# Optimization experiments

Measured on AMD Instinct MI355X. Metric: run time of the kernel, lower is better.

## Reference

```python
import jax, jax.numpy as jnp
import numpy as np

B, NSL, DS = 8, 12, 768
L, R, DL = 24, 64, 4096
DP = 4096
DIM_T = NSL * 2 * DS          # 18432
FUSED = 1024 + 512            # 1536
GEN_IN = FUSED + 256 + 64     # 1856


def setup_inputs() -> dict:
    key = jax.random.key(0)
    ks = jax.random.split(key, 16)
    s = lambda d: 1.0 / np.sqrt(d)
    return {
        "A_small": jax.random.normal(ks[0], (B, NSL, 1, DS), jnp.float32),
        "B_small": jax.random.normal(ks[1], (B, NSL, DS, 1), jnp.float32),
        "prompt_emb": jax.random.normal(ks[2], (B, DP), jnp.float32),
        "W_ct": jax.random.normal(ks[3], (DIM_T, 1024), jnp.float32) * s(DIM_T),
        "b_ct": jnp.zeros((1024,), jnp.float32),
        "W_cp": jax.random.normal(ks[4], (DP, 512), jnp.float32) * s(DP),
        "b_cp": jnp.zeros((512,), jnp.float32),
        "W_pc": jax.random.normal(ks[5], (FUSED, L), jnp.float32) * s(FUSED),
        "b_pc": jnp.zeros((L,), jnp.float32),
        "E_layer": jax.random.normal(ks[6], (L, 256), jnp.float32),
        "E_chunk": jax.random.normal(ks[7], (R, 64), jnp.float32),
        "W_A": jax.random.normal(ks[8], (GEN_IN, DL), jnp.float32) * s(GEN_IN),
        "b_A": jnp.zeros((DL,), jnp.float32),
        "W_B": jax.random.normal(ks[9], (GEN_IN, DL), jnp.float32) * s(GEN_IN),
        "b_B": jnp.zeros((DL,), jnp.float32),
    }


def reference(A_small, B_small, prompt_emb, W_ct, b_ct, W_cp, b_cp, W_pc, b_pc,
              E_layer, E_chunk, W_A, b_A, W_B, b_B):
    bsz = prompt_emb.shape[0]
    flat_T = jnp.concatenate([A_small.reshape(bsz, -1), B_small.reshape(bsz, -1)], axis=-1)
    t_feat = jax.nn.relu(flat_T @ W_ct + b_ct)          # [B,1024]
    p_feat = jax.nn.relu(prompt_emb @ W_cp + b_cp)      # [B,512]
    fused = jnp.concatenate([t_feat, p_feat], axis=-1)  # [B,1536]
    logits = fused @ W_pc + b_pc                        # [B,L]
    y_soft = jax.nn.sigmoid(logits)                     # eval mode (no gumbel)
    y_hard = (y_soft > 0.5).astype(y_soft.dtype)
    gate = y_soft + jax.lax.stop_gradient(y_hard - y_soft)  # straight-through

    # Batched hypernetwork over all (layer, chunk) pairs instead of a double loop.
    ctx = jnp.broadcast_to(fused[:, None, None, :], (bsz, L, R, FUSED))
    le = jnp.broadcast_to(E_layer[None, :, None, :], (bsz, L, R, 256))
    ce = jnp.broadcast_to(E_chunk[None, None, :, :], (bsz, L, R, 64))
    gen = jnp.concatenate([ctx, le, ce], axis=-1)       # [B,L,R,1856]

    A = gen @ W_A + b_A                                 # [B,L,R,DL]
    Bm = gen @ W_B + b_B                                # [B,L,R,DL]
    A_large = A * gate[:, :, None, None]                # [B,L,R,DL]
    B_large = jnp.transpose(Bm, (0, 1, 3, 2))           # [B,L,DL,R]
    return (A_large, B_large, gate)
```

## Files before the change

kernel.cpp:

```cpp
#include <hip/hip_runtime.h>

typedef float v4f __attribute__((ext_vector_type(4)));

#define NB 8
#define NL 24
#define NR 64
#define ND 4096
#define NFUSED 1536
#define NTF 1024
#define NPF 512
#define KP 4096

#define TKC 144
#define PKC 32
#define FKC 12

#define WS_FUSED 0
#define WS_GATE  12288
#define WS_PLA   12480
#define WS_PLB   209088
#define WS_CA    405696
#define WS_CBT   667840
#define WS_PT    929984
#define WS_PP    2109632
#define WS_PFA   2240704
#define WS_PFB   2633920

__global__ __launch_bounds__(256) void k_indep(
    const float* __restrict__ As, const float* __restrict__ Bs,
    const float* __restrict__ W_ct,
    const float* __restrict__ prompt, const float* __restrict__ W_cp,
    const float* __restrict__ E_layer, const float* __restrict__ E_chunk,
    const float* __restrict__ W_A, const float* __restrict__ W_B,
    float* __restrict__ partT, float* __restrict__ partP,
    float* __restrict__ pLA, float* __restrict__ pLB,
    float* __restrict__ CA, float* __restrict__ CBT) {
  __shared__ float e[NR * 64];
  const int bx = blockIdx.x;
  const int tid = threadIdx.x;

  if (bx < 576) {
    const int j = (bx & 3) * 256 + tid;
    const int kc = bx >> 2;
    const int kbase = kc * 128;
    float acc[NB] = {};
    for (int kk = 0; kk < 128; ++kk) {
      const int k = kbase + kk;
      const float w = W_ct[(size_t)k * NTF + j];
      const float* x = (k < 9216) ? (As + k) : (Bs + (k - 9216));
#pragma unroll
      for (int b = 0; b < NB; ++b) acc[b] = fmaf(x[b * 9216], w, acc[b]);
    }
#pragma unroll
    for (int b = 0; b < NB; ++b)
      partT[(size_t)(kc * NB + b) * NTF + j] = acc[b];
  } else if (bx < 640) {
    const int t = bx - 576;
    const int j = (t & 1) * 256 + tid;
    const int kc = t >> 1;
    const int kbase = kc * 128;
    float acc[NB] = {};
    for (int kk = 0; kk < 128; ++kk) {
      const int k = kbase + kk;
      const float w = W_cp[(size_t)k * NPF + j];
#pragma unroll
      for (int b = 0; b < NB; ++b) acc[b] = fmaf(prompt[b * KP + k], w, acc[b]);
    }
#pragma unroll
    for (int b = 0; b < NB; ++b)
      partP[(size_t)(kc * NB + b) * NPF + j] = acc[b];
  } else if (bx < 704) {
    const int t = bx - 640;
    const bool isA = t < 32;
    const int tt = isA ? t : t - 32;
    const int dc = tt & 15;
    const int kh = tt >> 4;
    const float* W = (isA ? W_A : W_B) + (size_t)(NFUSED + kh * 128) * ND;
    float* pL = (isA ? pLA : pLB) + (size_t)kh * NL * ND;
    const int d = dc * 256 + tid;
    float acc[NL] = {};
    for (int kk = 0; kk < 128; ++kk) {
      const float w = W[(size_t)kk * ND + d];
      const float* el = E_layer + kh * 128 + kk;
#pragma unroll
      for (int l = 0; l < NL; ++l) acc[l] = fmaf(el[l * 256], w, acc[l]);
    }
#pragma unroll
    for (int l = 0; l < NL; ++l) pL[(size_t)l * ND + d] = acc[l];
  } else {
    const int t = bx - 704;
    const bool isA = t < 16;
    const int tt = isA ? t : t - 16;
    const float* W = (isA ? W_A : W_B) + (size_t)(NFUSED + 256) * ND;
    for (int i = tid; i < NR * 64; i += 256) e[i] = E_chunk[i];
    __syncthreads();
    const int d = tt * 256 + tid;
    float w[64];
#pragma unroll
    for (int k = 0; k < 64; ++k) w[k] = W[(size_t)k * ND + d];
    for (int r = 0; r < NR; ++r) {
      float s = 0.f;
#pragma unroll
      for (int k = 0; k < 64; ++k) s = fmaf(e[r * 64 + k], w[k], s);
      if (isA) CA[(size_t)r * ND + d] = s;
      else     CBT[(size_t)d * NR + r] = s;
    }
  }
}

__global__ __launch_bounds__(256) void k_fused_reduce(
    const float* __restrict__ partT, const float* __restrict__ partP,
    const float* __restrict__ b_ct, const float* __restrict__ b_cp,
    float* __restrict__ fused) {
  const int bx = blockIdx.x;
  if (bx < 32) {
    const int idx = bx * 256 + threadIdx.x;
    const int b = idx >> 10, j = idx & 1023;
    float s = b_ct[j];
    for (int kc = 0; kc < TKC; ++kc) s += partT[(size_t)(kc * NB + b) * NTF + j];
    fused[b * NFUSED + j] = fmaxf(s, 0.f);
  } else {
    const int idx = (bx - 32) * 256 + threadIdx.x;
    const int b = idx >> 9, j = idx & 511;
    float s = b_cp[j];
    for (int kc = 0; kc < PKC; ++kc) s += partP[(size_t)(kc * NB + b) * NPF + j];
    fused[b * NFUSED + NTF + j] = fmaxf(s, 0.f);
  }
}

__global__ __launch_bounds__(256) void k_dep(
    const float* __restrict__ fused,
    const float* __restrict__ W_A, const float* __restrict__ W_B,
    const float* __restrict__ W_pc, const float* __restrict__ b_pc,
    float* __restrict__ pFA, float* __restrict__ pFB,
    float* __restrict__ gate_ws, float* __restrict__ gate_out) {
  __shared__ float red[256];
  const int bx = blockIdx.x;
  const int tid = threadIdx.x;
  if (bx < 384) {
    const bool isA = bx < 192;
    const int t = isA ? bx : bx - 192;
    const float* W = isA ? W_A : W_B;
    float* part = isA ? pFA : pFB;
    const int d = (t & 15) * 256 + tid;
    const int kc = t >> 4;
    const int kbase = kc * 128;
    float acc[NB] = {};
    for (int kk = 0; kk < 128; ++kk) {
      const int k = kbase + kk;
      const float w = W[(size_t)k * ND + d];
#pragma unroll
      for (int b = 0; b < NB; ++b) acc[b] = fmaf(fused[b * NFUSED + k], w, acc[b]);
    }
#pragma unroll
    for (int b = 0; b < NB; ++b)
      part[(size_t)(kc * NB + b) * ND + d] = acc[b];
  } else {
    const int bl = bx - 384;
    const int b = bl / NL, l = bl % NL;
    float s = 0.f;
    for (int k = tid; k < NFUSED; k += 256)
      s = fmaf(fused[b * NFUSED + k], W_pc[k * NL + l], s);
    red[tid] = s;
    __syncthreads();
#pragma unroll
    for (int off = 128; off > 0; off >>= 1) {
      if (tid < off) red[tid] += red[tid + off];
      __syncthreads();
    }
    if (tid == 0) {
      const float g = (red[0] + b_pc[l]) > 0.f ? 1.f : 0.f;
      gate_ws[bl] = g;
      gate_out[bl] = g;
    }
  }
}

__global__ __launch_bounds__(256) void k_out(
    const float* __restrict__ pFA, const float* __restrict__ pFB,
    const float* __restrict__ b_A, const float* __restrict__ b_B,
    const float* __restrict__ pLA, const float* __restrict__ pLB,
    const float* __restrict__ CA, const float* __restrict__ CBT,
    const float* __restrict__ gate,
    float* __restrict__ outA, float* __restrict__ outB) {
  __shared__ float sbase[512];
  const int bx = blockIdx.x;
  const int tid = threadIdx.x;
  if (bx < 1536) {
    const int bl = bx >> 3;
    const int rest = bx & 7;
    const int b = bl / NL, l = bl % NL;
    const int d = (rest >> 1) * 1024 + tid * 4;
    const int r0 = (rest & 1) * 32;
    const float g = gate[bl];
    v4f base = *(const v4f*)(b_A + d);
#pragma unroll
    for (int kc = 0; kc < FKC; ++kc)
      base += *(const v4f*)(pFA + (size_t)(kc * NB + b) * ND + d);
    base += *(const v4f*)(pLA + (size_t)l * ND + d);
    base += *(const v4f*)(pLA + (size_t)(NL + l) * ND + d);
    float* outp = outA + ((size_t)bl * NR + r0) * ND + d;
#pragma unroll 4
    for (int r = 0; r < 32; ++r) {
      const v4f c = *(const v4f*)(CA + (size_t)(r0 + r) * ND + d);
      const v4f v = (base + c) * g;
      __builtin_nontemporal_store(v, (v4f*)outp);
      outp += ND;
    }
  } else {
    const int t = bx - 1536;
    const int bl = t >> 3;
    const int b = bl / NL, l = bl % NL;
    const int dbase = (t & 7) * 512;
    for (int dd = tid; dd < 512; dd += 256) {
      const int d = dbase + dd;
      float s = b_B[d] + pLB[(size_t)l * ND + d] + pLB[(size_t)(NL + l) * ND + d];
#pragma unroll
      for (int kc = 0; kc < FKC; ++kc)
        s += pFB[(size_t)(kc * NB + b) * ND + d];
      sbase[dd] = s;
    }
    __syncthreads();
    const int dd16 = tid >> 4;
    const int r4 = (tid & 15) * 4;
#pragma unroll 4
    for (int i = 0; i < 32; ++i) {
      const int dloc = i * 16 + dd16;
      const int d = dbase + dloc;
      const v4f c = *(const v4f*)(CBT + (size_t)d * NR + r4);
      const v4f v = c + sbase[dloc];
      __builtin_nontemporal_store(v, (v4f*)(outB + ((size_t)bl * ND + d) * NR + r4));
    }
  }
}

extern "C" void kernel_launch(void* const* d_in, const int* in_sizes, int n_in,
                              void* d_out, int out_size, void* d_ws, size_t ws_size,
                              hipStream_t stream) {
  const float* A_small   = (const float*)d_in[0];
  const float* B_small   = (const float*)d_in[1];
  const float* prompt    = (const float*)d_in[2];
  const float* W_ct      = (const float*)d_in[3];
  const float* b_ct      = (const float*)d_in[4];
  const float* W_cp      = (const float*)d_in[5];
  const float* b_cp      = (const float*)d_in[6];
  const float* W_pc      = (const float*)d_in[7];
  const float* b_pc      = (const float*)d_in[8];
  const float* E_layer   = (const float*)d_in[9];
  const float* E_chunk   = (const float*)d_in[10];
  const float* W_A       = (const float*)d_in[11];
  const float* b_A       = (const float*)d_in[12];
  const float* W_B       = (const float*)d_in[13];
  const float* b_B       = (const float*)d_in[14];

  float* ws    = (float*)d_ws;
  float* fused = ws + WS_FUSED;
  float* gatew = ws + WS_GATE;
  float* pLA   = ws + WS_PLA;
  float* pLB   = ws + WS_PLB;
  float* CA    = ws + WS_CA;
  float* CBT   = ws + WS_CBT;
  float* partT = ws + WS_PT;
  float* partP = ws + WS_PP;
  float* pFA   = ws + WS_PFA;
  float* pFB   = ws + WS_PFB;

  float* outA = (float*)d_out;
  float* outB = outA + (size_t)192 * NR * ND;
  float* outG = outB + (size_t)192 * ND * NR;

  k_indep<<<736, 256, 0, stream>>>(A_small, B_small, W_ct, prompt, W_cp,
                                   E_layer, E_chunk, W_A, W_B,
                                   partT, partP, pLA, pLB, CA, CBT);
  k_fused_reduce<<<48, 256, 0, stream>>>(partT, partP, b_ct, b_cp, fused);
  k_dep<<<576, 256, 0, stream>>>(fused, W_A, W_B, W_pc, b_pc,
                                 pFA, pFB, gatew, outG);
  k_out<<<3072, 256, 0, stream>>>(pFA, pFB, b_A, b_B, pLA, pLB, CA, CBT,
                                  gatew, outA, outB);
}
```

Before: 151.5 us.

## Merge four kernels into one persistent cooperative kernel with grid syncs

Replaces the four separate kernel launches with a single cooperative persistent kernel. Each former kernel's block range becomes a grid-stride loop over work units, and grid.sync() separates the stages. This removes the launch gaps and inter-kernel drain between the stages. The cost is that the grid is capped by occupancy (at most 1024 blocks), each grid barrier carries overhead, and the launch_bounds(256,4) register cap may cause spills in the register-heavy stages.

Result: slower. 521.4 us (+244.2%).

```diff
diff --git a/kernel.cpp b/kernel.cpp
--- a/kernel.cpp
+++ b/kernel.cpp
@@ -1,4 +1,7 @@
 #include <hip/hip_runtime.h>
+#include <hip/hip_cooperative_groups.h>
+
+namespace cg = cooperative_groups;
 
 typedef float v4f __attribute__((ext_vector_type(4)));
 
@@ -26,210 +29,198 @@
 #define WS_PFA   2240704
 #define WS_PFB   2633920
 
-__global__ __launch_bounds__(256) void k_indep(
-    const float* __restrict__ As, const float* __restrict__ Bs,
-    const float* __restrict__ W_ct,
-    const float* __restrict__ prompt, const float* __restrict__ W_cp,
-    const float* __restrict__ E_layer, const float* __restrict__ E_chunk,
-    const float* __restrict__ W_A, const float* __restrict__ W_B,
-    float* __restrict__ partT, float* __restrict__ partP,
-    float* __restrict__ pLA, float* __restrict__ pLB,
-    float* __restrict__ CA, float* __restrict__ CBT) {
-  __shared__ float e[NR * 64];
-  const int bx = blockIdx.x;
+struct KParams {
+  const float *As, *Bs, *prompt, *W_ct, *b_ct, *W_cp, *b_cp, *W_pc, *b_pc,
+              *E_layer, *E_chunk, *W_A, *b_A, *W_B, *b_B;
+  float *fused, *gatew, *pLA, *pLB, *CA, *CBT, *partT, *partP, *pFA, *pFB;
+  float *outA, *outB, *outG;
+};
+
+__global__ __launch_bounds__(256, 4) void k_all(KParams p) {
+  cg::grid_group grid = cg::this_grid();
+  const int bid = blockIdx.x;
   const int tid = threadIdx.x;
-
-  if (bx < 576) {
-    const int j = (bx & 3) * 256 + tid;
-    const int kc = bx >> 2;
-    const int kbase = kc * 128;
-    float acc[NB] = {};
-    for (int kk = 0; kk < 128; ++kk) {
-      const int k = kbase + kk;
-      const float w = W_ct[(size_t)k * NTF + j];
-      const float* x = (k < 9216) ? (As + k) : (Bs + (k - 9216));
-#pragma unroll
-      for (int b = 0; b < NB; ++b) acc[b] = fmaf(x[b * 9216], w, acc[b]);
-    }
-#pragma unroll
-    for (int b = 0; b < NB; ++b)
-      partT[(size_t)(kc * NB + b) * NTF + j] = acc[b];
-  } else if (bx < 640) {
-    const int t = bx - 576;
-    const int j = (t & 1) * 256 + tid;
-    const int kc = t >> 1;
-    const int kbase = kc * 128;
-    float acc[NB] = {};
-    for (int kk = 0; kk < 128; ++kk) {
-      const int k = kbase + kk;
-      const float w = W_cp[(size_t)k * NPF + j];
-#pragma unroll
-      for (int b = 0; b < NB; ++b) acc[b] = fmaf(prompt[b * KP + k], w, acc[b]);
-    }
-#pragma unroll
-    for (int b = 0; b < NB; ++b)
-      partP[(size_t)(kc * NB + b) * NPF + j] = acc[b];
-  } else if (bx < 704) {
-    const int t = bx - 640;
-    const bool isA = t < 32;
-    const int tt = isA ? t : t - 32;
-    const int dc = tt & 15;
-    const int kh = tt >> 4;
-    const float* W = (isA ? W_A : W_B) + (size_t)(NFUSED + kh * 128) * ND;
-    float* pL = (isA ? pLA : pLB) + (size_t)kh * NL * ND;
-    const int d = dc * 256 + tid;
-    float acc[NL] = {};
-    for (int kk = 0; kk < 128; ++kk) {
-      const float w = W[(size_t)kk * ND + d];
-      const float* el = E_layer + kh * 128 + kk;
-#pragma unroll
-      for (int l = 0; l < NL; ++l) acc[l] = fmaf(el[l * 256], w, acc[l]);
-    }
-#pragma unroll
-    for (int l = 0; l < NL; ++l) pL[(size_t)l * ND + d] = acc[l];
-  } else {
-    const int t = bx - 704;
-    const bool isA = t < 16;
-    const int tt = isA ? t : t - 16;
-    const float* W = (isA ? W_A : W_B) + (size_t)(NFUSED + 256) * ND;
-    for (int i = tid; i < NR * 64; i += 256) e[i] = E_chunk[i];
-    __syncthreads();
-    const int d = tt * 256 + tid;
-    float w[64];
-#pragma unroll
-    for (int k = 0; k < 64; ++k) w[k] = W[(size_t)k * ND + d];
-    for (int r = 0; r < NR; ++r) {
+  const int G = gridDim.x;
+  __shared__ float smem[4096];
+
+  for (int u = bid; u < 736; u += G) {
+    if (u < 576) {
+      const int j = (u & 3) * 256 + tid;
+      const int kc = u >> 2;
+      const int kbase = kc * 128;
+      float acc[NB] = {};
+      for (int kk = 0; kk < 128; ++kk) {
+        const int k = kbase + kk;
+        const float w = p.W_ct[(size_t)k * NTF + j];
+        const float* x = (k < 9216) ? (p.As + k) : (p.Bs + (k - 9216));
+#pragma unroll
+        for (int b = 0; b < NB; ++b) acc[b] = fmaf(x[b * 9216], w, acc[b]);
+      }
+#pragma unroll
+      for (int b = 0; b < NB; ++b)
+        p.partT[(size_t)(kc * NB + b) * NTF + j] = acc[b];
+    } else if (u < 640) {
+      const int t = u - 576;
+      const int j = (t & 1) * 256 + tid;
+      const int kc = t >> 1;
+      const int kbase = kc * 128;
+      float acc[NB] = {};
+      for (int kk = 0; kk < 128; ++kk) {
+        const int k = kbase + kk;
+        const float w = p.W_cp[(size_t)k * NPF + j];
+#pragma unroll
+        for (int b = 0; b < NB; ++b) acc[b] = fmaf(p.prompt[b * KP + k], w, acc[b]);
+      }
+#pragma unroll
+      for (int b = 0; b < NB; ++b)
+        p.partP[(size_t)(kc * NB + b) * NPF + j] = acc[b];
+    } else if (u < 704) {
+      const int t = u - 640;
+      const bool isA = t < 32;
+      const int tt = isA ? t : t - 32;
+      const int dc = tt & 15;
+      const int kh = tt >> 4;
+      const float* W = (isA ? p.W_A : p.W_B) + (size_t)(NFUSED + kh * 128) * ND;
+      float* pL = (isA ? p.pLA : p.pLB) + (size_t)kh * NL * ND;
+      const int d = dc * 256 + tid;
+      float acc[NL] = {};
+      for (int kk = 0; kk < 128; ++kk) {
+        const float w = W[(size_t)kk * ND + d];
+        const float* el = p.E_layer + kh * 128 + kk;
+#pragma unroll
+        for (int l = 0; l < NL; ++l) acc[l] = fmaf(el[l * 256], w, acc[l]);
+      }
+#pragma unroll
+      for (int l = 0; l < NL; ++l) pL[(size_t)l * ND + d] = acc[l];
+    } else {
+      const int t = u - 704;
+      const bool isA = t < 16;
+      const int tt = isA ? t : t - 16;
+      const float* W = (isA ? p.W_A : p.W_B) + (size_t)(NFUSED + 256) * ND;
+      __syncthreads();
+      for (int i = tid; i < NR * 64; i += 256) smem[i] = p.E_chunk[i];
+      __syncthreads();
+      const int d = tt * 256 + tid;
+      float w[64];
+#pragma unroll
+      for (int k = 0; k < 64; ++k) w[k] = W[(size_t)k * ND + d];
+      for (int r = 0; r < NR; ++r) {
+        float s = 0.f;
+#pragma unroll
+        for (int k = 0; k < 64; ++k) s = fmaf(smem[r * 64 + k], w[k], s);
+        if (isA) p.CA[(size_t)r * ND + d] = s;
+        else     p.CBT[(size_t)d * NR + r] = s;
+      }
+    }
+  }
+  grid.sync();
+
+  for (int u = bid; u < 48; u += G) {
+    if (u < 32) {
+      const int idx = u * 256 + tid;
+      const int b = idx >> 10, j = idx & 1023;
+      float s = p.b_ct[j];
+      for (int kc = 0; kc < TKC; ++kc) s += p.partT[(size_t)(kc * NB + b) * NTF + j];
+      p.fused[b * NFUSED + j] = fmaxf(s, 0.f);
+    } else {
+      const int idx = (u - 32) * 256 + tid;
+      const int b = idx >> 9, j = idx & 511;
+      float s = p.b_cp[j];
+      for (int kc = 0; kc < PKC; ++kc) s += p.partP[(size_t)(kc * NB + b) * NPF + j];
+      p.fused[b * NFUSED + NTF + j] = fmaxf(s, 0.f);
+    }
+  }
+  grid.sync();
+
+  for (int u = bid; u < 576; u += G) {
+    if (u < 384) {
+      const bool isA = u < 192;
+      const int t = isA ? u : u - 192;
+      const float* W = isA ? p.W_A : p.W_B;
+      float* part = isA ? p.pFA : p.pFB;
+      const int d = (t & 15) * 256 + tid;
+      const int kc = t >> 4;
+      const int kbase = kc * 128;
+      float acc[NB] = {};
+      for (int kk = 0; kk < 128; ++kk) {
+        const int k = kbase + kk;
+        const float w = W[(size_t)k * ND + d];
+#pragma unroll
+        for (int b = 0; b < NB; ++b) acc[b] = fmaf(p.fused[b * NFUSED + k], w, acc[b]);
+      }
+#pragma unroll
+      for (int b = 0; b < NB; ++b)
+        part[(size_t)(kc * NB + b) * ND + d] = acc[b];
+    } else {
+      const int bl = u - 384;
+      const int b = bl / NL, l = bl % NL;
       float s = 0.f;
-#pragma unroll
-      for (int k = 0; k < 64; ++k) s = fmaf(e[r * 64 + k], w[k], s);
-      if (isA) CA[(size_t)r * ND + d] = s;
-      else     CBT[(size_t)d * NR + r] = s;
-    }
-  }
-}
-
-__global__ __launch_bounds__(256) void k_fused_reduce(
-    const float* __restrict__ partT, const float* __restrict__ partP,
-    const float* __restrict__ b_ct, const float* __restrict__ b_cp,
-    float* __restrict__ fused) {
-  const int bx = blockIdx.x;
-  if (bx < 32) {
-    const int idx = bx * 256 + threadIdx.x;
-    const int b = idx >> 10, j = idx & 1023;
-    float s = b_ct[j];
-    for (int kc = 0; kc < TKC; ++kc) s += partT[(size_t)(kc * NB + b) * NTF + j];
-    fused[b * NFUSED + j] = fmaxf(s, 0.f);
-  } else {
-    const int idx = (bx - 32) * 256 + threadIdx.x;
-    const int b = idx >> 9, j = idx & 511;
-    float s = b_cp[j];
-    for (int kc = 0; kc < PKC; ++kc) s += partP[(size_t)(kc * NB + b) * NPF + j];
-    fused[b * NFUSED + NTF + j] = fmaxf(s, 0.f);
-  }
-}
-
-__global__ __launch_bounds__(256) void k_dep(
-    const float* __restrict__ fused,
-    const float* __restrict__ W_A, const float* __restrict__ W_B,
-    const float* __restrict__ W_pc, const float* __restrict__ b_pc,
-    float* __restrict__ pFA, float* __restrict__ pFB,
-    float* __restrict__ gate_ws, float* __restrict__ gate_out) {
-  __shared__ float red[256];
-  const int bx = blockIdx.x;
-  const int tid = threadIdx.x;
-  if (bx < 384) {
-    const bool isA = bx < 192;
-    const int t = isA ? bx : bx - 192;
-    const float* W = isA ? W_A : W_B;
-    float* part = isA ? pFA : pFB;
-    const int d = (t & 15) * 256 + tid;
-    const int kc = t >> 4;
-    const int kbase = kc * 128;
-    float acc[NB] = {};
-    for (int kk = 0; kk < 128; ++kk) {
-      const int k = kbase + kk;
-      const float w = W[(size_t)k * ND + d];
-#pragma unroll
-      for (int b = 0; b < NB; ++b) acc[b] = fmaf(fused[b * NFUSED + k], w, acc[b]);
-    }
-#pragma unroll
-    for (int b = 0; b < NB; ++b)
-      part[(size_t)(kc * NB + b) * ND + d] = acc[b];
-  } else {
-    const int bl = bx - 384;
-    const int b = bl / NL, l = bl % NL;
-    float s = 0.f;
-    for (int k = tid; k < NFUSED; k += 256)
-      s = fmaf(fused[b * NFUSED + k], W_pc[k * NL + l], s);
-    red[tid] = s;
-    __syncthreads();
-#pragma unroll
-    for (int off = 128; off > 0; off >>= 1) {
-      if (tid < off) red[tid] += red[tid + off];
-      __syncthreads();
-    }
-    if (tid == 0) {
-      const float g = (red[0] + b_pc[l]) > 0.f ? 1.f : 0.f;
-      gate_ws[bl] = g;
-      gate_out[bl] = g;
-    }
-  }
-}
-
-__global__ __launch_bounds__(256) void k_out(
-    const float* __restrict__ pFA, const float* __restrict__ pFB,
-    const float* __restrict__ b_A, const float* __restrict__ b_B,
-    const float* __restrict__ pLA, const float* __restrict__ pLB,
-    const float* __restrict__ CA, const float* __restrict__ CBT,
-    const float* __restrict__ gate,
-    float* __restrict__ outA, float* __restrict__ outB) {
-  __shared__ float sbase[512];
-  const int bx = blockIdx.x;
-  const int tid = threadIdx.x;
-  if (bx < 1536) {
-    const int bl = bx >> 3;
-    const int rest = bx & 7;
-    const int b = bl / NL, l = bl % NL;
-    const int d = (rest >> 1) * 1024 + tid * 4;
-    const int r0 = (rest & 1) * 32;
-    const float g = gate[bl];
-    v4f base = *(const v4f*)(b_A + d);
-#pragma unroll
-    for (int kc = 0; kc < FKC; ++kc)
-      base += *(const v4f*)(pFA + (size_t)(kc * NB + b) * ND + d);
-    base += *(const v4f*)(pLA + (size_t)l * ND + d);
-    base += *(const v4f*)(pLA + (size_t)(NL + l) * ND + d);
-    float* outp = outA + ((size_t)bl * NR + r0) * ND + d;
+      for (int k = tid; k < NFUSED; k += 256)
+        s = fmaf(p.fused[b * NFUSED + k], p.W_pc[k * NL + l], s);
+      __syncthreads();
+      smem[tid] = s;
+      __syncthreads();
+#pragma unroll
+      for (int off = 128; off > 0; off >>= 1) {
+        if (tid < off) smem[tid] += smem[tid + off];
+        __syncthreads();
+      }
+      if (tid == 0) {
+        const float g = (smem[0] + p.b_pc[l]) > 0.f ? 1.f : 0.f;
+        p.gatew[bl] = g;
+        p.outG[bl] = g;
+      }
+    }
+  }
+  grid.sync();
+
+  for (int u = bid; u < 3072; u += G) {
+    if (u < 1536) {
+      const int bl = u >> 3;
+      const int rest = u & 7;
+      const int b = bl / NL, l = bl % NL;
+      const int d = (rest >> 1) * 1024 + tid * 4;
+      const int r0 = (rest & 1) * 32;
+      const float g = p.gatew[bl];
+      v4f base = *(const v4f*)(p.b_A + d);
+#pragma unroll
+      for (int kc = 0; kc < FKC; ++kc)
+        base += *(const v4f*)(p.pFA + (size_t)(kc * NB + b) * ND + d);
+      base += *(const v4f*)(p.pLA + (size_t)l * ND + d);
+      base += *(const v4f*)(p.pLA + (size_t)(NL + l) * ND + d);
+      float* outp = p.outA + ((size_t)bl * NR + r0) * ND + d;
 #pragma unroll 4
-    for (int r = 0; r < 32; ++r) {
-      const v4f c = *(const v4f*)(CA + (size_t)(r0 + r) * ND + d);
-      const v4f v = (base + c) * g;
-      __builtin_nontemporal_store(v, (v4f*)outp);
-      outp += ND;
-    }
-  } else {
-    const int t = bx - 1536;
-    const int bl = t >> 3;
-    const int b = bl / NL, l = bl % NL;
-    const int dbase = (t & 7) * 512;
-    for (int dd = tid; dd < 512; dd += 256) {
-      const int d = dbase + dd;
-      float s = b_B[d] + pLB[(size_t)l * ND + d] + pLB[(size_t)(NL + l) * ND + d];
-#pragma unroll
-      for (int kc = 0; kc < FKC; ++kc)
-        s += pFB[(size_t)(kc * NB + b) * ND + d];
-      sbase[dd] = s;
-    }
-    __syncthreads();
-    const int dd16 = tid >> 4;
-    const int r4 = (tid & 15) * 4;
+      for (int r = 0; r < 32; ++r) {
+        const v4f c = *(const v4f*)(p.CA + (size_t)(r0 + r) * ND + d);
+        const v4f v = (base + c) * g;
+        __builtin_nontemporal_store(v, (v4f*)outp);
+        outp += ND;
+      }
+    } else {
+      const int t = u - 1536;
+      const int bl = t >> 3;
+      const int b = bl / NL, l = bl % NL;
+      const int dbase = (t & 7) * 512;
+      __syncthreads();
+      for (int dd = tid; dd < 512; dd += 256) {
+        const int d = dbase + dd;
+        float s = p.b_B[d] + p.pLB[(size_t)l * ND + d] + p.pLB[(size_t)(NL + l) * ND + d];
+#pragma unroll
+        for (int kc = 0; kc < FKC; ++kc)
+          s += p.pFB[(size_t)(kc * NB + b) * ND + d];
+        smem[dd] = s;
+      }
+      __syncthreads();
+      const int dd16 = tid >> 4;
+      const int r4 = (tid & 15) * 4;
 #pragma unroll 4
-    for (int i = 0; i < 32; ++i) {
-      const int dloc = i * 16 + dd16;
-      const int d = dbase + dloc;
-      const v4f c = *(const v4f*)(CBT + (size_t)d * NR + r4);
-      const v4f v = c + sbase[dloc];
-      __builtin_nontemporal_store(v, (v4f*)(outB + ((size_t)bl * ND + d) * NR + r4));
+      for (int i = 0; i < 32; ++i) {
+        const int dloc = i * 16 + dd16;
+        const int d = dbase + dloc;
+        const v4f c = *(const v4f*)(p.CBT + (size_t)d * NR + r4);
+        const v4f v = c + smem[dloc];
+        __builtin_nontemporal_store(v, (v4f*)(p.outB + ((size_t)bl * ND + d) * NR + r4));
+      }
     }
   }
 }
@@ -237,44 +228,49 @@
 extern "C" void kernel_launch(void* const* d_in, const int* in_sizes, int n_in,
                               void* d_out, int out_size, void* d_ws, size_t ws_size,
                               hipStream_t stream) {
-  const float* A_small   = (const float*)d_in[0];
-  const float* B_small   = (const float*)d_in[1];
-  const float* prompt    = (const float*)d_in[2];
-  const float* W_ct      = (const float*)d_in[3];
-  const float* b_ct      = (const float*)d_in[4];
-  const float* W_cp      = (const float*)d_in[5];
-  const float* b_cp      = (const float*)d_in[6];
-  const float* W_pc      = (const float*)d_in[7];
-  const float* b_pc      = (const float*)d_in[8];
-  const float* E_layer   = (const float*)d_in[9];
-  const float* E_chunk   = (const float*)d_in[10];
-  const float* W_A       = (const float*)d_in[11];
-  const float* b_A       = (const float*)d_in[12];
-  const float* W_B       = (const float*)d_in[13];
-  const float* b_B       = (const float*)d_in[14];
-
-  float* ws    = (float*)d_ws;
-  float* fused = ws + WS_FUSED;
-  float* gatew = ws + WS_GATE;
-  float* pLA   = ws + WS_PLA;
-  float* pLB   = ws + WS_PLB;
-  float* CA    = ws + WS_CA;
-  float* CBT   = ws + WS_CBT;
-  float* partT = ws + WS_PT;
-  float* partP = ws + WS_PP;
-  float* pFA   = ws + WS_PFA;
-  float* pFB   = ws + WS_PFB;
-
+  float* ws = (float*)d_ws;
   float* outA = (float*)d_out;
   float* outB = outA + (size_t)192 * NR * ND;
   float* outG = outB + (size_t)192 * ND * NR;
 
-  k_indep<<<736, 256, 0, stream>>>(A_small, B_small, W_ct, prompt, W_cp,
-                                   E_layer, E_chunk, W_A, W_B,
-                                   partT, partP, pLA, pLB, CA, CBT);
-  k_fused_reduce<<<48, 256, 0, stream>>>(partT, partP, b_ct, b_cp, fused);
-  k_dep<<<576, 256, 0, stream>>>(fused, W_A, W_B, W_pc, b_pc,
-                                 pFA, pFB, gatew, outG);
-  k_out<<<3072, 256, 0, stream>>>(pFA, pFB, b_A, b_B, pLA, pLB, CA, CBT,
-                                  gatew, outA, outB);
+  KParams p;
+  p.As      = (const float*)d_in[0];
+  p.Bs      = (const float*)d_in[1];
+  p.prompt  = (const float*)d_in[2];
+  p.W_ct    = (const float*)d_in[3];
+  p.b_ct    = (const float*)d_in[4];
+  p.W_cp    = (const float*)d_in[5];
+  p.b_cp    = (const float*)d_in[6];
+  p.W_pc    = (const float*)d_in[7];
+  p.b_pc    = (const float*)d_in[8];
+  p.E_layer = (const float*)d_in[9];
+  p.E_chunk = (const float*)d_in[10];
+  p.W_A     = (const float*)d_in[11];
+  p.b_A     = (const float*)d_in[12];
+  p.W_B     = (const float*)d_in[13];
+  p.b_B     = (const float*)d_in[14];
+  p.fused   = ws + WS_FUSED;
+  p.gatew   = ws + WS_GATE;
+  p.pLA     = ws + WS_PLA;
+  p.pLB     = ws + WS_PLB;
+  p.CA      = ws + WS_CA;
+  p.CBT     = ws + WS_CBT;
+  p.partT   = ws + WS_PT;
+  p.partP   = ws + WS_PP;
+  p.pFA     = ws + WS_PFA;
+  p.pFB     = ws + WS_PFB;
+  p.outA    = outA;
+  p.outB    = outB;
+  p.outG    = outG;
+
+  int maxb = 0;
+  (void)hipOccupancyMaxActiveBlocksPerMultiprocessor(
+      &maxb, reinterpret_cast<const void*>(k_all), 256, 0);
+  if (maxb < 1) maxb = 1;
+  long grid = (long)maxb * 256;
+  if (grid > 1024) grid = 1024;
+
+  void* args[] = {&p};
+  (void)hipLaunchCooperativeKernel(reinterpret_cast<const void*>(k_all),
+                                   dim3((int)grid), dim3(256), args, 0, stream);
 }
```

## Fuse fused-feature reduction into dependent GEMV kernel and batch gate computation

Applied to the files above, without the earlier changes.

Removes the separate k_fused_reduce launch. Each k_dep block now reduces the partial sums for its own 128-wide k-slice of the fused features into shared memory, and the GEMV reads from there. The gate blocks drop from 192 (one per batch,layer) to 8 (one per batch): each rebuilds the full fused vector in shared memory and computes all 24 logits with wave shuffles. This saves a launch and a global round trip, but every k_dep block repeats reduction work over partT (each slice is recomputed by 16 d-chunk blocks), and the gate blocks do a long serial reduction.

Result: slower. 166.9 us (+10.2%).

```diff
diff --git a/kernel.cpp b/kernel.cpp
--- a/kernel.cpp
+++ b/kernel.cpp
@@ -15,7 +15,6 @@
 #define PKC 32
 #define FKC 12
 
-#define WS_FUSED 0
 #define WS_GATE  12288
 #define WS_PLA   12480
 #define WS_PLB   209088
@@ -108,70 +107,101 @@
   }
 }
 
-__global__ __launch_bounds__(256) void k_fused_reduce(
+__global__ __launch_bounds__(256) void k_dep(
     const float* __restrict__ partT, const float* __restrict__ partP,
     const float* __restrict__ b_ct, const float* __restrict__ b_cp,
-    float* __restrict__ fused) {
-  const int bx = blockIdx.x;
-  if (bx < 32) {
-    const int idx = bx * 256 + threadIdx.x;
-    const int b = idx >> 10, j = idx & 1023;
-    float s = b_ct[j];
-    for (int kc = 0; kc < TKC; ++kc) s += partT[(size_t)(kc * NB + b) * NTF + j];
-    fused[b * NFUSED + j] = fmaxf(s, 0.f);
-  } else {
-    const int idx = (bx - 32) * 256 + threadIdx.x;
-    const int b = idx >> 9, j = idx & 511;
-    float s = b_cp[j];
-    for (int kc = 0; kc < PKC; ++kc) s += partP[(size_t)(kc * NB + b) * NPF + j];
-    fused[b * NFUSED + NTF + j] = fmaxf(s, 0.f);
-  }
-}
-
-__global__ __launch_bounds__(256) void k_dep(
-    const float* __restrict__ fused,
     const float* __restrict__ W_A, const float* __restrict__ W_B,
     const float* __restrict__ W_pc, const float* __restrict__ b_pc,
     float* __restrict__ pFA, float* __restrict__ pFB,
     float* __restrict__ gate_ws, float* __restrict__ gate_out) {
-  __shared__ float red[256];
+  __shared__ float smem[1664];
   const int bx = blockIdx.x;
   const int tid = threadIdx.x;
+
   if (bx < 384) {
     const bool isA = bx < 192;
     const int t = isA ? bx : bx - 192;
     const float* W = isA ? W_A : W_B;
     float* part = isA ? pFA : pFB;
-    const int d = (t & 15) * 256 + tid;
+    const int dc = t & 15;
     const int kc = t >> 4;
-    const int kbase = kc * 128;
+
+    const int j = tid & 127;
+    const int bhalf = tid >> 7;
+    if (kc < 8) {
+      const int gj = kc * 128 + j;
+      const float bias = b_ct[gj];
+#pragma unroll
+      for (int p4 = 0; p4 < 4; ++p4) {
+        const int b = p4 * 2 + bhalf;
+        float s = bias;
+        for (int kcc = 0; kcc < TKC; ++kcc)
+          s += partT[(size_t)(kcc * NB + b) * NTF + gj];
+        smem[b * 128 + j] = fmaxf(s, 0.f);
+      }
+    } else {
+      const int jj = kc * 128 - NTF + j;
+      const float bias = b_cp[jj];
+#pragma unroll
+      for (int p4 = 0; p4 < 4; ++p4) {
+        const int b = p4 * 2 + bhalf;
+        float s = bias;
+        for (int kcc = 0; kcc < PKC; ++kcc)
+          s += partP[(size_t)(kcc * NB + b) * NPF + jj];
+        smem[b * 128 + j] = fmaxf(s, 0.f);
+      }
+    }
+    __syncthreads();
+
+    const int d = dc * 256 + tid;
     float acc[NB] = {};
     for (int kk = 0; kk < 128; ++kk) {
-      const int k = kbase + kk;
-      const float w = W[(size_t)k * ND + d];
-#pragma unroll
-      for (int b = 0; b < NB; ++b) acc[b] = fmaf(fused[b * NFUSED + k], w, acc[b]);
+      const float w = W[(size_t)(kc * 128 + kk) * ND + d];
+#pragma unroll
+      for (int b = 0; b < NB; ++b) acc[b] = fmaf(smem[b * 128 + kk], w, acc[b]);
     }
 #pragma unroll
     for (int b = 0; b < NB; ++b)
       part[(size_t)(kc * NB + b) * ND + d] = acc[b];
   } else {
-    const int bl = bx - 384;
-    const int b = bl / NL, l = bl % NL;
-    float s = 0.f;
-    for (int k = tid; k < NFUSED; k += 256)
-      s = fmaf(fused[b * NFUSED + k], W_pc[k * NL + l], s);
-    red[tid] = s;
-    __syncthreads();
-#pragma unroll
-    for (int off = 128; off > 0; off >>= 1) {
-      if (tid < off) red[tid] += red[tid + off];
-      __syncthreads();
-    }
-    if (tid == 0) {
-      const float g = (red[0] + b_pc[l]) > 0.f ? 1.f : 0.f;
-      gate_ws[bl] = g;
-      gate_out[bl] = g;
+    const int b = bx - 384;
+    for (int j = tid; j < NFUSED; j += 256) {
+      float s;
+      if (j < NTF) {
+        s = b_ct[j];
+        for (int kc = 0; kc < TKC; ++kc)
+          s += partT[(size_t)(kc * NB + b) * NTF + j];
+      } else {
+        const int jj = j - NTF;
+        s = b_cp[jj];
+        for (int kc = 0; kc < PKC; ++kc)
+          s += partP[(size_t)(kc * NB + b) * NPF + jj];
+      }
+      smem[j] = fmaxf(s, 0.f);
+    }
+    __syncthreads();
+    float acc[NL] = {};
+    for (int j = tid; j < NFUSED; j += 256) {
+      const float f = smem[j];
+#pragma unroll
+      for (int l = 0; l < NL; ++l) acc[l] = fmaf(f, W_pc[j * NL + l], acc[l]);
+    }
+#pragma unroll
+    for (int off = 32; off > 0; off >>= 1)
+#pragma unroll
+      for (int l = 0; l < NL; ++l) acc[l] += __shfl_down(acc[l], off);
+    const int wave = tid >> 6, lane = tid & 63;
+    if (lane == 0)
+#pragma unroll
+      for (int l = 0; l < NL; ++l) smem[NFUSED + wave * NL + l] = acc[l];
+    __syncthreads();
+    if (tid < NL) {
+      float s = b_pc[tid];
+#pragma unroll
+      for (int w = 0; w < 4; ++w) s += smem[NFUSED + w * NL + tid];
+      const float g = s > 0.f ? 1.f : 0.f;
+      gate_ws[b * NL + tid] = g;
+      gate_out[b * NL + tid] = g;
     }
   }
 }
@@ -254,7 +284,6 @@
   const float* b_B       = (const float*)d_in[14];
 
   float* ws    = (float*)d_ws;
-  float* fused = ws + WS_FUSED;
   float* gatew = ws + WS_GATE;
   float* pLA   = ws + WS_PLA;
   float* pLB   = ws + WS_PLB;
@@ -272,9 +301,8 @@
   k_indep<<<736, 256, 0, stream>>>(A_small, B_small, W_ct, prompt, W_cp,
                                    E_layer, E_chunk, W_A, W_B,
                                    partT, partP, pLA, pLB, CA, CBT);
-  k_fused_reduce<<<48, 256, 0, stream>>>(partT, partP, b_ct, b_cp, fused);
-  k_dep<<<576, 256, 0, stream>>>(fused, W_A, W_B, W_pc, b_pc,
-                                 pFA, pFB, gatew, outG);
+  k_dep<<<392, 256, 0, stream>>>(partT, partP, b_ct, b_cp, W_A, W_B,
+                                 W_pc, b_pc, pFA, pFB, gatew, outG);
   k_out<<<3072, 256, 0, stream>>>(pFA, pFB, b_A, b_B, pLA, pLB, CA, CBT,
                                   gatew, outA, outB);
 }
```
